# Kernel tuning notes

Measured on AMD Instinct MI355X. Metric: run time of the kernel, lower is better.

## Reference

```python
import jax, jax.numpy as jnp
import numpy as np

B, S, E, H = 4, 4096, 1024, 16
D = E // H  # head_dim = 64
EPS = 1e-6


def setup_inputs() -> dict:
    key = jax.random.key(0)
    ks = jax.random.split(key, 11)
    inv = 1.0 / np.sqrt(E)
    return {
        "query": jax.random.normal(ks[0], (B, S, E), dtype=jnp.float32),
        "key": jax.random.normal(ks[1], (B, S, E), dtype=jnp.float32),
        "value": jax.random.normal(ks[2], (B, S, E), dtype=jnp.float32),
        "key_padding_mask": jnp.zeros((B, S), dtype=bool),
        "Wq": jax.random.uniform(ks[3], (E, E), jnp.float32, -inv, inv),
        "bq": jnp.zeros((E,), jnp.float32),
        "Wk": jax.random.uniform(ks[4], (E, E), jnp.float32, -inv, inv),
        "bk": jnp.zeros((E,), jnp.float32),
        "Wv": jax.random.uniform(ks[5], (E, E), jnp.float32, -inv, inv),
        "bv": jnp.zeros((E,), jnp.float32),
        "Wo": jax.random.uniform(ks[6], (E, E), jnp.float32, -inv, inv),
        "bo": jnp.zeros((E,), jnp.float32),
    }


def _heads(x):
    # (B,S,E) -> (B,H,S,D)
    return x.reshape(B, -1, H, D).transpose(0, 2, 1, 3)


def reference(query, key, value, key_padding_mask, Wq, bq, Wk, bk, Wv, bv, Wo, bo):
    q = _heads(query @ Wq.T + bq)
    k = _heads(key @ Wk.T + bk)
    v = _heads(value @ Wv.T + bv)

    q_aug = jax.nn.relu(q) + EPS
    k_aug = jax.nn.relu(k) + EPS
    # mask out padded keys: (B,S_k) -> (B,1,S_k,1)
    k_aug = jnp.where(key_padding_mask[:, None, :, None], 0.0, k_aug)

    kv_context = jnp.einsum("bhsd,bhsv->bhdv", k_aug, v)  # (B,H,D,D)
    k_sum = k_aug.sum(axis=2)                                # (B,H,D)
    denom = jnp.einsum("bhqd,bhd->bhq", q_aug, k_sum)
    denom = jnp.maximum(denom, EPS)

    attn = jnp.einsum("bhqd,bhdv->bhqv", q_aug, kv_context) / denom[..., None]
    attn = attn.transpose(0, 2, 1, 3).reshape(B, -1, E)      # (B,S_q,E)
    # dropout is identity in eval mode
    return attn @ Wo.T + bo
```

## Files before the change

kernel.cpp:

```cpp
#include <hip/hip_runtime.h>
#include <hip/hip_bf16.h>
#include <stdint.h>

#define B_ 4
#define S_ 4096
#define E_ 1024
#define H_ 16
#define D_ 64
#define M_ (B_*S_)
constexpr float kEPS = 1e-6f;

typedef unsigned short u16;
typedef unsigned char  u8;
typedef __bf16 bf16x8 __attribute__((ext_vector_type(8)));
typedef float  f32x4  __attribute__((ext_vector_type(4)));
typedef u16    u16x8  __attribute__((ext_vector_type(8)));

typedef const __attribute__((address_space(1))) void* gaddr_t;
typedef __attribute__((address_space(3))) void*       laddr_t;

__device__ __forceinline__ u16 f2bf(float f) {
    union { float f; uint32_t u; } v; v.f = f;
    uint32_t u = v.u;
    u += 0x7fffu + ((u >> 16) & 1u);
    return (u16)(u >> 16);
}
__device__ __forceinline__ float hi2f(uint32_t d) {
    union { uint32_t u; float f; } v; v.u = d & 0xffff0000u;
    return v.f;
}
__device__ __forceinline__ float lo2f(uint32_t d) {
    union { uint32_t u; float f; } v; v.u = d << 16;
    return v.f;
}

#define VM_WAIT(n) asm volatile("s_waitcnt vmcnt(" #n ")" ::: "memory")
#define LG0        asm volatile("s_waitcnt lgkmcnt(0)" ::: "memory")
#define SBAR       asm volatile("s_barrier" ::: "memory")

__global__ void cvt_kernel(const float* __restrict__ in, u16* __restrict__ out, int n4) {
    int i = blockIdx.x * blockDim.x + threadIdx.x;
    if (i >= n4) return;
    float4 v = reinterpret_cast<const float4*>(in)[i];
    ushort4 o;
    o.x = f2bf(v.x); o.y = f2bf(v.y); o.z = f2bf(v.z); o.w = f2bf(v.w);
    reinterpret_cast<ushort4*>(out)[i] = o;
}

#define BM 256
#define BN 256
#define BKT 64
#define NKT (E_/BKT)

template<int EPI>
__global__ __launch_bounds__(512, 2)
void gemm8(const u16* __restrict__ A, const u16* __restrict__ Bw,
           const float* __restrict__ bias, const u8* __restrict__ mask,
           float* __restrict__ Cf, u16* __restrict__ Cb)
{
    extern __shared__ u16 lds[];
    const int tid  = threadIdx.x;
    const int wid  = tid >> 6, lane = tid & 63;
    const int wqr  = wid >> 2, wqc = wid & 3;
    const int m0   = blockIdx.x * BM;
    const int n0   = blockIdx.y * BN;
    const int fr   = lane & 15;
    const int cg   = lane >> 4;

    const int srow = tid >> 3;
    const int ssc  = tid & 7;
    const int sck  = ssc ^ (srow & 7);
    const u16* aS = A  + (size_t)(m0 + srow)*E_ + sck*8;
    const u16* bS = Bw + (size_t)(n0 + srow)*E_ + sck*8;
    const int sd0 = tid*8, sd1 = (tid + 512)*8;

    int arow[4], brow[2];
#pragma unroll
    for (int mf = 0; mf < 4; ++mf) arow[mf] = (wqr*64 + mf*16 + fr) * 64;
#pragma unroll
    for (int nf = 0; nf < 2; ++nf) brow[nf] = (wqc*32 + nf*16 + fr) * 64;
    const int kx0 = ((cg)     ^ (fr & 7)) * 8;
    const int kx1 = ((4 + cg) ^ (fr & 7)) * 8;

    f32x4 acc[2][2][4][2] = {};
    bf16x8 afr[4][2];

    float bias_v[2][2];
#pragma unroll
    for (int nh = 0; nh < 2; ++nh)
#pragma unroll
        for (int nf = 0; nf < 2; ++nf)
            bias_v[nh][nf] = bias[n0 + nh*128 + wqc*32 + nf*16 + fr];

#define STAGE(BUF, MAT, H, T) do { \
        u16* dst_ = lds + (BUF)*32768 + (MAT)*16384 + (H)*8192; \
        const u16* src_ = ((MAT) ? bS : aS) + (size_t)(H)*128*E_ + (size_t)(T)*BKT; \
        __builtin_amdgcn_global_load_lds((gaddr_t)(src_),                  (laddr_t)(dst_ + sd0), 16, 0, 0); \
        __builtin_amdgcn_global_load_lds((gaddr_t)(src_ + (size_t)64*E_), (laddr_t)(dst_ + sd1), 16, 0, 0); \
    } while (0)

#define PH(BUF, MH, NH, STG_STMT, WAIT_STMT) do { \
        const u16* Ab_ = lds + (BUF)*32768 + (MH)*8192; \
        const u16* Bb_ = lds + (BUF)*32768 + 16384 + (NH)*8192; \
        if ((NH) == 0) { \
            _Pragma("unroll") \
            for (int mf_ = 0; mf_ < 4; ++mf_) { \
                afr[mf_][0] = *reinterpret_cast<const bf16x8*>(Ab_ + arow[mf_] + kx0); \
                afr[mf_][1] = *reinterpret_cast<const bf16x8*>(Ab_ + arow[mf_] + kx1); \
            } \
        } \
        bf16x8 bfv[2][2]; \
        _Pragma("unroll") \
        for (int nf_ = 0; nf_ < 2; ++nf_) { \
            bfv[nf_][0] = *reinterpret_cast<const bf16x8*>(Bb_ + brow[nf_] + kx0); \
            bfv[nf_][1] = *reinterpret_cast<const bf16x8*>(Bb_ + brow[nf_] + kx1); \
        } \
        STG_STMT; \
        WAIT_STMT; \
        SBAR; \
        LG0; \
        __builtin_amdgcn_sched_barrier(0); \
        __builtin_amdgcn_s_setprio(1); \
        _Pragma("unroll") \
        for (int mf_ = 0; mf_ < 4; ++mf_) { \
            _Pragma("unroll") \
            for (int nf_ = 0; nf_ < 2; ++nf_) { \
                acc[MH][NH][mf_][nf_] = __builtin_amdgcn_mfma_f32_16x16x32_bf16(afr[mf_][0], bfv[nf_][0], acc[MH][NH][mf_][nf_], 0, 0, 0); \
                acc[MH][NH][mf_][nf_] = __builtin_amdgcn_mfma_f32_16x16x32_bf16(afr[mf_][1], bfv[nf_][1], acc[MH][NH][mf_][nf_], 0, 0, 0); \
            } \
        } \
        __builtin_amdgcn_s_setprio(0); \
        SBAR; \
    } while (0)

    STAGE(0, 0, 0, 0);
    STAGE(0, 1, 0, 0);
    STAGE(0, 0, 1, 0);
    STAGE(0, 1, 1, 0);
    STAGE(1, 0, 0, 1);
    STAGE(1, 1, 0, 1);
    VM_WAIT(4);
    SBAR;
    __builtin_amdgcn_sched_barrier(0);

#pragma unroll 1
    for (int i = 0; i < 7; ++i) {
        const int T1 = 2*i + 1, T2 = 2*i + 2, T3 = 2*i + 3;
        PH(0, 0, 0, STAGE(1, 0, 1, T1), ;);
        PH(0, 0, 1, STAGE(1, 1, 1, T1), ;);
        PH(0, 1, 0, STAGE(0, 0, 0, T2), ;);
        PH(0, 1, 1, STAGE(0, 1, 0, T2), VM_WAIT(4));
        PH(1, 0, 0, STAGE(0, 0, 1, T2), ;);
        PH(1, 0, 1, STAGE(0, 1, 1, T2), ;);
        PH(1, 1, 0, STAGE(1, 0, 0, T3), ;);
        PH(1, 1, 1, STAGE(1, 1, 0, T3), VM_WAIT(4));
    }
    PH(0, 0, 0, STAGE(1, 0, 1, 15), ;);
    PH(0, 0, 1, STAGE(1, 1, 1, 15), ;);
    PH(0, 1, 0, ;, ;);
    PH(0, 1, 1, ;, VM_WAIT(0));
    PH(1, 0, 0, ;, ;);
    PH(1, 0, 1, ;, ;);
    PH(1, 1, 0, ;, ;);
    PH(1, 1, 1, ;, ;);
#undef PH
#undef STAGE

    const int bblk = m0 >> 12;
    const int sloc = m0 & 4095;
#pragma unroll
    for (int mh = 0; mh < 2; ++mh) {
#pragma unroll
    for (int nh = 0; nh < 2; ++nh) {
#pragma unroll
    for (int mf = 0; mf < 4; ++mf) {
#pragma unroll
        for (int nf = 0; nf < 2; ++nf) {
            const int gn = n0 + nh*128 + wqc*32 + nf*16 + fr;
            const int mb = mh*128 + wqr*64 + mf*16 + cg*4;
            if (EPI == 2 || EPI == 3) {
                ushort4 o;
#pragma unroll
                for (int r = 0; r < 4; ++r) {
                    float x = acc[mh][nh][mf][nf][r] + bias_v[nh][nf];
                    if (EPI == 2) {
                        x = fmaxf(x, 0.f) + kEPS;
                        if (mask[m0 + mb + r]) x = 0.f;
                    }
                    ((u16*)&o)[r] = f2bf(x);
                }
                *reinterpret_cast<ushort4*>(Cb + ((size_t)(bblk*1024 + gn))*4096 + sloc + mb) = o;
            } else {
#pragma unroll
                for (int r = 0; r < 4; ++r) {
                    const int gm = m0 + mb + r;
                    float x = acc[mh][nh][mf][nf][r] + bias_v[nh][nf];
                    if (EPI == 0) {
                        Cf[(size_t)gm*E_ + gn] = x;
                    } else {
                        x = fmaxf(x, 0.f) + kEPS;
                        Cb[(size_t)gm*E_ + gn] = f2bf(x);
                    }
                }
            }
        }
    }
    }
    }
}

#define NSC 8
#define KCH (S_/NSC)
__global__ __launch_bounds__(256)
void kv_mfma_kernel(const u16* __restrict__ KaT, const u16* __restrict__ VvT,
                    float* __restrict__ kvp, float* __restrict__ ksp)
{
    __shared__ float sm[4][64];
    const int bh = blockIdx.x, sc = blockIdx.y;
    const int tid = threadIdx.x;
    const int w = tid >> 6, lane = tid & 63;
    const int fr = lane & 15, cg = lane >> 4;

    const u16* Ar = VvT + ((size_t)bh*64 + w*16 + fr)*4096 + sc*KCH;
    const u16* Br0 = KaT + ((size_t)bh*64 + fr)*4096 + sc*KCH;

    f32x4 acc[4] = {};
#pragma unroll 2
    for (int ks = 0; ks < KCH/32; ++ks) {
        const int ko = ks*32 + cg*8;
        bf16x8 af = *reinterpret_cast<const bf16x8*>(Ar + ko);
#pragma unroll
        for (int nf = 0; nf < 4; ++nf) {
            bf16x8 bf = *reinterpret_cast<const bf16x8*>(Br0 + (size_t)nf*16*4096 + ko);
            acc[nf] = __builtin_amdgcn_mfma_f32_16x16x32_bf16(af, bf, acc[nf], 0, 0, 0);
        }
    }
    float* dst = kvp + ((size_t)sc*64 + bh)*4096;
#pragma unroll
    for (int nf = 0; nf < 4; ++nf)
#pragma unroll
        for (int r = 0; r < 4; ++r)
            dst[(w*16 + cg*4 + r)*64 + nf*16 + fr] = acc[nf][r];

    {
        const int d = tid & 63, qq = tid >> 6;
        const u16* kr = KaT + ((size_t)bh*64 + d)*4096 + sc*KCH + qq*(KCH/4);
        float s = 0.f;
#pragma unroll 4
        for (int i = 0; i < KCH/4/8; ++i) {
            bf16x8 kk = *reinterpret_cast<const bf16x8*>(kr + i*8);
#pragma unroll
            for (int j = 0; j < 8; ++j) s += (float)kk[j];
        }
        sm[qq][d] = s;
    }
    __syncthreads();
    if (tid < 64)
        ksp[((size_t)sc*64 + bh)*64 + tid] = sm[0][tid] + sm[1][tid] + sm[2][tid] + sm[3][tid];
}

__global__ __launch_bounds__(256)
void kv_reduce_kernel(const float* __restrict__ kvp, const float* __restrict__ ksp,
                      u16* __restrict__ kvT, float* __restrict__ ksum)
{
    const int i = blockIdx.x*256 + threadIdx.x;
    float s = 0.f;
#pragma unroll
    for (int c = 0; c < NSC; ++c) s += kvp[(size_t)c*262144 + i];
    kvT[i] = f2bf(s);
    if (i < 4096) {
        float t = 0.f;
#pragma unroll
        for (int c = 0; c < NSC; ++c) t += ksp[(size_t)c*4096 + i];
        ksum[i] = t;
    }
}

__global__ __launch_bounds__(256)
void attn_kernel(const u16* __restrict__ Qa, const u16* __restrict__ kvT,
                 const float* __restrict__ ksum, u16* __restrict__ attn)
{
    __shared__ u16  Qs[256*64];
    __shared__ u16  Ts[64*64];
    __shared__ float kss[64];
    __shared__ float invd[256];

    const int bh = blockIdx.x, b = bh >> 4, h = bh & 15;
    const int s0 = blockIdx.y * 256;
    const int tid = threadIdx.x;
    const int wid = tid >> 6, lane = tid & 63;
    const int fr = lane & 15, cg = lane >> 4;

#pragma unroll
    for (int j = 0; j < 8; ++j) {
        int L = (wid*8 + j)*64 + lane;
        int row = L >> 3, c = L & 7;
        int cs = c ^ (row & 7);
        const u16* src = Qa + (size_t)(b*S_ + s0 + row)*E_ + h*64 + cs*8;
        __builtin_amdgcn_global_load_lds((gaddr_t)src, (laddr_t)(Qs + L*8), 16, 0, 0);
    }
#pragma unroll
    for (int k = 0; k < 2; ++k) {
        int g = k*256 + tid;
        int v = g >> 3, c = g & 7;
        uint4 q = *reinterpret_cast<const uint4*>(kvT + (size_t)bh*4096 + g*8);
        int cs = c ^ (v & 7);
        *reinterpret_cast<uint4*>(Ts + v*64 + cs*8) = q;
    }
    if (tid < 64) kss[tid] = ksum[bh*64 + tid];
    asm volatile("s_waitcnt vmcnt(0) lgkmcnt(0)" ::: "memory");
    __syncthreads();

    {
        float den = 0.f;
#pragma unroll
        for (int c = 0; c < 8; ++c) {
            uint4 qc = *reinterpret_cast<const uint4*>(Qs + tid*64 + (c ^ (tid & 7))*8);
            den += lo2f(qc.x)*kss[c*8+0] + hi2f(qc.x)*kss[c*8+1]
                 + lo2f(qc.y)*kss[c*8+2] + hi2f(qc.y)*kss[c*8+3]
                 + lo2f(qc.z)*kss[c*8+4] + hi2f(qc.z)*kss[c*8+5]
                 + lo2f(qc.w)*kss[c*8+6] + hi2f(qc.w)*kss[c*8+7];
        }
        invd[tid] = 1.0f / fmaxf(den, kEPS);
    }
    __syncthreads();

    f32x4 acc[4][4] = {};
#pragma unroll
    for (int ks = 0; ks < 2; ++ks) {
        bf16x8 bfrag[4];
#pragma unroll
        for (int nf = 0; nf < 4; ++nf) {
            int v = nf*16 + fr;
            bfrag[nf] = *reinterpret_cast<const bf16x8*>(Ts + v*64 + ((ks*4 + cg) ^ (v & 7))*8);
        }
#pragma unroll
        for (int mf = 0; mf < 4; ++mf) {
            int m = wid*64 + mf*16 + fr;
            bf16x8 afrag = *reinterpret_cast<const bf16x8*>(Qs + m*64 + ((ks*4 + cg) ^ (m & 7))*8);
#pragma unroll
            for (int nf = 0; nf < 4; ++nf)
                acc[mf][nf] = __builtin_amdgcn_mfma_f32_16x16x32_bf16(afrag, bfrag[nf], acc[mf][nf], 0, 0, 0);
        }
    }

#pragma unroll
    for (int mf = 0; mf < 4; ++mf) {
#pragma unroll
        for (int nf = 0; nf < 4; ++nf) {
            const int v = nf*16 + fr;
#pragma unroll
            for (int r = 0; r < 4; ++r) {
                const int row = wid*64 + mf*16 + cg*4 + r;
                float x = acc[mf][nf][r] * invd[row];
                attn[(size_t)(b*S_ + s0 + row)*E_ + h*64 + v] = f2bf(x);
            }
        }
    }
}

extern "C" void kernel_launch(void* const* d_in, const int* in_sizes, int n_in,
                              void* d_out, int out_size, void* d_ws, size_t ws_size,
                              hipStream_t stream)
{
    const float* query = (const float*)d_in[0];
    const float* key   = (const float*)d_in[1];
    const float* value = (const float*)d_in[2];
    const u8*    mask  = (const u8*)d_in[3];
    const float* Wq = (const float*)d_in[4];
    const float* bq = (const float*)d_in[5];
    const float* Wk = (const float*)d_in[6];
    const float* bk = (const float*)d_in[7];
    const float* Wv = (const float*)d_in[8];
    const float* bv = (const float*)d_in[9];
    const float* Wo = (const float*)d_in[10];
    const float* bo = (const float*)d_in[11];
    float* out = (float*)d_out;

    const size_t SZ_ME = (size_t)M_ * E_;
    const size_t SZ_EE = (size_t)E_ * E_;

    char* ws = (char*)d_ws;
    u16* qx   = (u16*)ws; ws += SZ_ME*2;
    u16* kx   = (u16*)ws; ws += SZ_ME*2;
    u16* vx   = (u16*)ws; ws += SZ_ME*2;
    u16* Qa   = (u16*)ws; ws += SZ_ME*2;
    u16* KaT  = (u16*)ws; ws += SZ_ME*2;
    u16* VvT  = (u16*)ws; ws += SZ_ME*2;
    u16* wqb  = (u16*)ws; ws += SZ_EE*2;
    u16* wkb  = (u16*)ws; ws += SZ_EE*2;
    u16* wvb  = (u16*)ws; ws += SZ_EE*2;
    u16* wob  = (u16*)ws; ws += SZ_EE*2;

    u16*   attnb = qx;
    float* kvp   = (float*)kx;
    float* ksp   = (float*)vx;
    u16*   kvT   = (u16*)((char*)vx + (size_t)NSC*4096*4);
    float* ksum  = (float*)((char*)kvT + (size_t)64*4096*2);

    cvt_kernel<<<(int)(SZ_ME/4/256), 256, 0, stream>>>(query, qx, (int)(SZ_ME/4));
    cvt_kernel<<<(int)(SZ_ME/4/256), 256, 0, stream>>>(key,   kx, (int)(SZ_ME/4));
    cvt_kernel<<<(int)(SZ_ME/4/256), 256, 0, stream>>>(value, vx, (int)(SZ_ME/4));
    cvt_kernel<<<(int)(SZ_EE/4/256), 256, 0, stream>>>(Wq, wqb, (int)(SZ_EE/4));
    cvt_kernel<<<(int)(SZ_EE/4/256), 256, 0, stream>>>(Wk, wkb, (int)(SZ_EE/4));
    cvt_kernel<<<(int)(SZ_EE/4/256), 256, 0, stream>>>(Wv, wvb, (int)(SZ_EE/4));
    cvt_kernel<<<(int)(SZ_EE/4/256), 256, 0, stream>>>(Wo, wob, (int)(SZ_EE/4));

    dim3 ggrid(M_/BM, E_/BN);
    constexpr size_t LDS_BYTES = 2 * 32768 * sizeof(u16);
    gemm8<1><<<ggrid, 512, LDS_BYTES, stream>>>(qx, wqb, bq, nullptr, nullptr, Qa);
    gemm8<2><<<ggrid, 512, LDS_BYTES, stream>>>(kx, wkb, bk, mask,    nullptr, KaT);
    gemm8<3><<<ggrid, 512, LDS_BYTES, stream>>>(vx, wvb, bv, nullptr, nullptr, VvT);

    kv_mfma_kernel<<<dim3(64, NSC), 256, 0, stream>>>(KaT, VvT, kvp, ksp);
    kv_reduce_kernel<<<1024, 256, 0, stream>>>(kvp, ksp, kvT, ksum);

    attn_kernel<<<dim3(B_*H_, S_/256), 256, 0, stream>>>(Qa, kvT, ksum, attnb);

    gemm8<0><<<ggrid, 512, LDS_BYTES, stream>>>(attnb, wob, bo, nullptr, out, nullptr);
}
```

Measured before the change: 266.7 us.

## Fuse fp32-to-bf16 activation conversion into QKV projection GEMM A-tile staging

Drops the three separate conversion kernels for query/key/value. The projection GEMMs now load fp32 A tiles into registers, convert them to bf16 and write them swizzled into LDS, overlapped with MFMA phases through a reworked software pipeline. This removes a full write and read of three bf16 activation copies. In exchange the A path goes through registers instead of direct global-to-LDS loads, which adds VGPR pressure and conversion work inside the main loop. The workspace layout is also reorganised.

```diff
diff --git a/kernel.cpp b/kernel.cpp
--- a/kernel.cpp
+++ b/kernel.cpp
@@ -52,9 +52,12 @@
 #define BKT 64
 #define NKT (E_/BKT)
 
-template<int EPI>
+struct ARegs { f32x4 r0, r1, r2, r3; };
+
+template<int EPI, bool AF32>
 __global__ __launch_bounds__(512, 2)
-void gemm8(const u16* __restrict__ A, const u16* __restrict__ Bw,
+void gemm8(const float* __restrict__ Af, const u16* __restrict__ Abf,
+           const u16* __restrict__ Bw,
            const float* __restrict__ bias, const u8* __restrict__ mask,
            float* __restrict__ Cf, u16* __restrict__ Cb)
 {
@@ -70,9 +73,14 @@
     const int srow = tid >> 3;
     const int ssc  = tid & 7;
     const int sck  = ssc ^ (srow & 7);
-    const u16* aS = A  + (size_t)(m0 + srow)*E_ + sck*8;
     const u16* bS = Bw + (size_t)(n0 + srow)*E_ + sck*8;
+    const u16* aS = (AF32 ? (const u16*)Af : Abf) + (size_t)(m0 + srow)*E_ + sck*8;
     const int sd0 = tid*8, sd1 = (tid + 512)*8;
+
+    const int ar  = tid >> 2;
+    const int ac4 = tid & 3;
+    const int aw0 = (2*ac4)     ^ (ar & 7);
+    const int aw1 = (2*ac4 + 1) ^ (ar & 7);
 
     int arow[4], brow[2];
 #pragma unroll
@@ -84,6 +92,7 @@
 
     f32x4 acc[2][2][4][2] = {};
     bf16x8 afr[4][2];
+    ARegs Ra, Rb;
 
     float bias_v[2][2];
 #pragma unroll
@@ -92,9 +101,36 @@
         for (int nf = 0; nf < 2; ++nf)
             bias_v[nh][nf] = bias[n0 + nh*128 + wqc*32 + nf*16 + fr];
 
-#define STAGE(BUF, MAT, H, T) do { \
-        u16* dst_ = lds + (BUF)*32768 + (MAT)*16384 + (H)*8192; \
-        const u16* src_ = ((MAT) ? bS : aS) + (size_t)(H)*128*E_ + (size_t)(T)*BKT; \
+#define AISSUE(REG, T, HH) do { \
+        const float* p_ = Af + (size_t)(m0 + (HH)*128 + ar)*E_ + (T)*BKT + ac4*16; \
+        REG.r0 = *reinterpret_cast<const f32x4*>(p_); \
+        REG.r1 = *reinterpret_cast<const f32x4*>(p_ + 4); \
+        REG.r2 = *reinterpret_cast<const f32x4*>(p_ + 8); \
+        REG.r3 = *reinterpret_cast<const f32x4*>(p_ + 12); \
+    } while (0)
+
+#define AWRITE(REG, BUF, HH) do { \
+        bf16x8 h0_, h1_; \
+        _Pragma("unroll") \
+        for (int j_ = 0; j_ < 4; ++j_) { \
+            h0_[j_]   = (__bf16)REG.r0[j_]; h0_[4+j_] = (__bf16)REG.r1[j_]; \
+            h1_[j_]   = (__bf16)REG.r2[j_]; h1_[4+j_] = (__bf16)REG.r3[j_]; \
+        } \
+        u16* d_ = lds + (BUF)*32768 + (HH)*8192 + ar*64; \
+        *reinterpret_cast<bf16x8*>(d_ + aw0*8) = h0_; \
+        *reinterpret_cast<bf16x8*>(d_ + aw1*8) = h1_; \
+    } while (0)
+
+#define BSTG(BUF, HH, T) do { \
+        u16* dst_ = lds + (BUF)*32768 + 16384 + (HH)*8192; \
+        const u16* src_ = bS + (size_t)(HH)*128*E_ + (size_t)(T)*BKT; \
+        __builtin_amdgcn_global_load_lds((gaddr_t)(src_),                  (laddr_t)(dst_ + sd0), 16, 0, 0); \
+        __builtin_amdgcn_global_load_lds((gaddr_t)(src_ + (size_t)64*E_), (laddr_t)(dst_ + sd1), 16, 0, 0); \
+    } while (0)
+
+#define ASTG(BUF, HH, T) do { \
+        u16* dst_ = lds + (BUF)*32768 + (HH)*8192; \
+        const u16* src_ = aS + (size_t)(HH)*128*E_ + (size_t)(T)*BKT; \
         __builtin_amdgcn_global_load_lds((gaddr_t)(src_),                  (laddr_t)(dst_ + sd0), 16, 0, 0); \
         __builtin_amdgcn_global_load_lds((gaddr_t)(src_ + (size_t)64*E_), (laddr_t)(dst_ + sd1), 16, 0, 0); \
     } while (0)
@@ -133,38 +169,76 @@
         SBAR; \
     } while (0)
 
-    STAGE(0, 0, 0, 0);
-    STAGE(0, 1, 0, 0);
-    STAGE(0, 0, 1, 0);
-    STAGE(0, 1, 1, 0);
-    STAGE(1, 0, 0, 1);
-    STAGE(1, 1, 0, 1);
-    VM_WAIT(4);
-    SBAR;
-    __builtin_amdgcn_sched_barrier(0);
+    if constexpr (AF32) {
+        AISSUE(Ra, 0, 0); AISSUE(Rb, 0, 1);
+        VM_WAIT(0);
+        AWRITE(Ra, 0, 0); AWRITE(Rb, 0, 1);
+        BSTG(0, 0, 0); BSTG(0, 1, 0);
+        AISSUE(Ra, 1, 0);
+        VM_WAIT(0);
+        AWRITE(Ra, 1, 0);
+        BSTG(1, 0, 1);
+        AISSUE(Rb, 1, 1);
+        SBAR;
+        __builtin_amdgcn_sched_barrier(0);
 
 #pragma unroll 1
-    for (int i = 0; i < 7; ++i) {
-        const int T1 = 2*i + 1, T2 = 2*i + 2, T3 = 2*i + 3;
-        PH(0, 0, 0, STAGE(1, 0, 1, T1), ;);
-        PH(0, 0, 1, STAGE(1, 1, 1, T1), ;);
-        PH(0, 1, 0, STAGE(0, 0, 0, T2), ;);
-        PH(0, 1, 1, STAGE(0, 1, 0, T2), VM_WAIT(4));
-        PH(1, 0, 0, STAGE(0, 0, 1, T2), ;);
-        PH(1, 0, 1, STAGE(0, 1, 1, T2), ;);
-        PH(1, 1, 0, STAGE(1, 0, 0, T3), ;);
-        PH(1, 1, 1, STAGE(1, 1, 0, T3), VM_WAIT(4));
-    }
-    PH(0, 0, 0, STAGE(1, 0, 1, 15), ;);
-    PH(0, 0, 1, STAGE(1, 1, 1, 15), ;);
-    PH(0, 1, 0, ;, ;);
-    PH(0, 1, 1, ;, VM_WAIT(0));
-    PH(1, 0, 0, ;, ;);
-    PH(1, 0, 1, ;, ;);
-    PH(1, 1, 0, ;, ;);
-    PH(1, 1, 1, ;, ;);
+        for (int i = 0; i < 7; ++i) {
+            const int T1 = 2*i + 1, T2 = 2*i + 2, T3 = 2*i + 3;
+            PH(0, 0, 0, AISSUE(Ra, T2, 0), { VM_WAIT(4); AWRITE(Rb, 1, 1); });
+            PH(0, 0, 1, BSTG(1, 1, T1), ;);
+            PH(0, 1, 0, AISSUE(Rb, T2, 1), { VM_WAIT(6); AWRITE(Ra, 0, 0); });
+            PH(0, 1, 1, BSTG(0, 0, T2), ;);
+            PH(1, 0, 0, AISSUE(Ra, T3, 0), { VM_WAIT(6); AWRITE(Rb, 0, 1); });
+            PH(1, 0, 1, BSTG(0, 1, T2), ;);
+            PH(1, 1, 0, AISSUE(Rb, T3, 1), { VM_WAIT(6); AWRITE(Ra, 1, 0); });
+            PH(1, 1, 1, BSTG(1, 0, T3), ;);
+        }
+        PH(0, 0, 0, ;, { VM_WAIT(0); AWRITE(Rb, 1, 1); });
+        PH(0, 0, 1, BSTG(1, 1, 15), ;);
+        PH(0, 1, 0, ;, ;);
+        PH(0, 1, 1, ;, ;);
+        PH(1, 0, 0, ;, VM_WAIT(0));
+        PH(1, 0, 1, ;, ;);
+        PH(1, 1, 0, ;, ;);
+        PH(1, 1, 1, ;, ;);
+    } else {
+        ASTG(0, 0, 0);
+        BSTG(0, 0, 0);
+        ASTG(0, 1, 0);
+        BSTG(0, 1, 0);
+        ASTG(1, 0, 1);
+        BSTG(1, 0, 1);
+        VM_WAIT(4);
+        SBAR;
+        __builtin_amdgcn_sched_barrier(0);
+
+#pragma unroll 1
+        for (int i = 0; i < 7; ++i) {
+            const int T1 = 2*i + 1, T2 = 2*i + 2, T3 = 2*i + 3;
+            PH(0, 0, 0, ASTG(1, 1, T1), ;);
+            PH(0, 0, 1, BSTG(1, 1, T1), ;);
+            PH(0, 1, 0, ASTG(0, 0, T2), ;);
+            PH(0, 1, 1, BSTG(0, 0, T2), VM_WAIT(4));
+            PH(1, 0, 0, ASTG(0, 1, T2), ;);
+            PH(1, 0, 1, BSTG(0, 1, T2), ;);
+            PH(1, 1, 0, ASTG(1, 0, T3), ;);
+            PH(1, 1, 1, BSTG(1, 0, T3), VM_WAIT(4));
+        }
+        PH(0, 0, 0, ASTG(1, 1, 15), ;);
+        PH(0, 0, 1, BSTG(1, 1, 15), ;);
+        PH(0, 1, 0, ;, ;);
+        PH(0, 1, 1, ;, VM_WAIT(0));
+        PH(1, 0, 0, ;, ;);
+        PH(1, 0, 1, ;, ;);
+        PH(1, 1, 0, ;, ;);
+        PH(1, 1, 1, ;, ;);
+    }
 #undef PH
-#undef STAGE
+#undef ASTG
+#undef BSTG
+#undef AWRITE
+#undef AISSUE
 
     const int bblk = m0 >> 12;
     const int sloc = m0 & 4095;
@@ -381,26 +455,19 @@
     const size_t SZ_EE = (size_t)E_ * E_;
 
     char* ws = (char*)d_ws;
-    u16* qx   = (u16*)ws; ws += SZ_ME*2;
-    u16* kx   = (u16*)ws; ws += SZ_ME*2;
-    u16* vx   = (u16*)ws; ws += SZ_ME*2;
     u16* Qa   = (u16*)ws; ws += SZ_ME*2;
     u16* KaT  = (u16*)ws; ws += SZ_ME*2;
     u16* VvT  = (u16*)ws; ws += SZ_ME*2;
+    u16* attnb= (u16*)ws; ws += SZ_ME*2;
     u16* wqb  = (u16*)ws; ws += SZ_EE*2;
     u16* wkb  = (u16*)ws; ws += SZ_EE*2;
     u16* wvb  = (u16*)ws; ws += SZ_EE*2;
     u16* wob  = (u16*)ws; ws += SZ_EE*2;
-
-    u16*   attnb = qx;
-    float* kvp   = (float*)kx;
-    float* ksp   = (float*)vx;
-    u16*   kvT   = (u16*)((char*)vx + (size_t)NSC*4096*4);
-    float* ksum  = (float*)((char*)kvT + (size_t)64*4096*2);
-
-    cvt_kernel<<<(int)(SZ_ME/4/256), 256, 0, stream>>>(query, qx, (int)(SZ_ME/4));
-    cvt_kernel<<<(int)(SZ_ME/4/256), 256, 0, stream>>>(key,   kx, (int)(SZ_ME/4));
-    cvt_kernel<<<(int)(SZ_ME/4/256), 256, 0, stream>>>(value, vx, (int)(SZ_ME/4));
+    float* kvp = (float*)ws; ws += (size_t)NSC*64*4096*4;
+    float* ksp = (float*)ws; ws += (size_t)NSC*4096*4;
+    u16*  kvT  = (u16*)ws;  ws += (size_t)64*4096*2;
+    float* ksum= (float*)ws; ws += 4096*4;
+
     cvt_kernel<<<(int)(SZ_EE/4/256), 256, 0, stream>>>(Wq, wqb, (int)(SZ_EE/4));
     cvt_kernel<<<(int)(SZ_EE/4/256), 256, 0, stream>>>(Wk, wkb, (int)(SZ_EE/4));
     cvt_kernel<<<(int)(SZ_EE/4/256), 256, 0, stream>>>(Wv, wvb, (int)(SZ_EE/4));
@@ -408,14 +475,14 @@
 
     dim3 ggrid(M_/BM, E_/BN);
     constexpr size_t LDS_BYTES = 2 * 32768 * sizeof(u16);
-    gemm8<1><<<ggrid, 512, LDS_BYTES, stream>>>(qx, wqb, bq, nullptr, nullptr, Qa);
-    gemm8<2><<<ggrid, 512, LDS_BYTES, stream>>>(kx, wkb, bk, mask,    nullptr, KaT);
-    gemm8<3><<<ggrid, 512, LDS_BYTES, stream>>>(vx, wvb, bv, nullptr, nullptr, VvT);
+    gemm8<1, true><<<ggrid, 512, LDS_BYTES, stream>>>(query, nullptr, wqb, bq, nullptr, nullptr, Qa);
+    gemm8<2, true><<<ggrid, 512, LDS_BYTES, stream>>>(key,   nullptr, wkb, bk, mask,    nullptr, KaT);
+    gemm8<3, true><<<ggrid, 512, LDS_BYTES, stream>>>(value, nullptr, wvb, bv, nullptr, nullptr, VvT);
 
     kv_mfma_kernel<<<dim3(64, NSC), 256, 0, stream>>>(KaT, VvT, kvp, ksp);
     kv_reduce_kernel<<<1024, 256, 0, stream>>>(kvp, ksp, kvT, ksum);
 
     attn_kernel<<<dim3(B_*H_, S_/256), 256, 0, stream>>>(Qa, kvT, ksum, attnb);
 
-    gemm8<0><<<ggrid, 512, LDS_BYTES, stream>>>(attnb, wob, bo, nullptr, out, nullptr);
-}
+    gemm8<0, false><<<ggrid, 512, LDS_BYTES, stream>>>(nullptr, attnb, wob, bo, nullptr, out, nullptr);
+}
```

Result: slower. 290.6 us (+9.0%).
